# Kernel optimization log

Hardware: AMD Instinct MI355X
Metric: run time of the kernel (lower is better)

Reference implementation:

```python
import jax, jax.numpy as jnp
import numpy as np

N_NODES = 100000
N_EDGES = 3200000
IN_DIM, HID, OUT_DIM = 512, 64, 5


def _glorot(key, shape):
    fan_in, fan_out = shape[0], shape[1]
    lim = np.sqrt(6.0 / (fan_in + fan_out))
    return jax.random.uniform(key, shape, jnp.float32, -lim, lim)


def setup_inputs() -> dict:
    key = jax.random.key(0)
    ks = jax.random.split(key, 10)
    x = jax.random.normal(ks[0], (N_NODES, IN_DIM), jnp.float32)
    edge_index = jax.random.randint(ks[1], (2, N_EDGES), 0, N_NODES, jnp.int64)
    edge_weight = jax.random.uniform(ks[2], (N_EDGES,), jnp.float32)
    return {
        "x": x,
        "edge_index": edge_index,
        "edge_weight": edge_weight,
        "W1": _glorot(ks[3], (IN_DIM, HID)),
        "b1": jnp.zeros((HID,), jnp.float32),
        "W2": _glorot(ks[4], (HID, HID)),
        "b2": jnp.zeros((HID,), jnp.float32),
        "Wfc": _glorot(ks[5], (HID, OUT_DIM)),
        "bfc": jnp.zeros((OUT_DIM,), jnp.float32),
    }


def _gcn_norm(edge_index, edge_weight, num_nodes):
    # PyG gcn_norm: add self-loops (weight 1), symmetric deg^-1/2 normalization.
    loop = jnp.arange(num_nodes, dtype=edge_index.dtype)
    src = jnp.concatenate([edge_index[0], loop])
    dst = jnp.concatenate([edge_index[1], loop])
    ew = jnp.concatenate([edge_weight, jnp.ones((num_nodes,), edge_weight.dtype)])
    deg = jax.ops.segment_sum(ew, dst, num_segments=num_nodes)
    dinv = jnp.where(deg > 0, jax.lax.rsqrt(deg), 0.0)
    norm = dinv[src] * ew * dinv[dst]
    return src, dst, norm


def _gcn_conv(x, W, b, src, dst, norm, num_nodes):
    h = x @ W  # transform first (GCNConv does lin before propagate)
    msg = norm[:, None] * h[src]  # gather + scale  [E, d]
    out = jax.ops.segment_sum(msg, dst, num_segments=num_nodes)  # scatter-add
    return out + b


def reference(x, edge_index, edge_weight, W1, b1, W2, b2, Wfc, bfc):
    n = x.shape[0]
    src, dst, norm = _gcn_norm(edge_index, edge_weight, n)
    h = jax.nn.relu(_gcn_conv(x, W1, b1, src, dst, norm, n))
    h = jax.nn.relu(_gcn_conv(h, W2, b2, src, dst, norm, n))
    return h @ Wfc + bfc
```

## Files before the change

### kernel.cpp

```cpp
#include <hip/hip_runtime.h>

#define IN_DIM 512
#define HID 64
#define OUT_DIM 5


__device__ __forceinline__ unsigned short f2bf(float f) {
    unsigned u = __float_as_uint(f);
    u += 0x7FFF + ((u >> 16) & 1);
    return (unsigned short)(u >> 16);
}
__device__ __forceinline__ float bf2f(unsigned short b) {
    return __uint_as_float(((unsigned)b) << 16);
}


__global__ void k_init(unsigned long long* __restrict__ packed, int n) {
    int i = blockIdx.x * blockDim.x + threadIdx.x;
    if (i < n) packed[i] = 0ULL;
}


__global__ void k_hist4(const int* __restrict__ dst, const float* __restrict__ ew,
                        unsigned long long* __restrict__ packed, int* __restrict__ rank, int nE) {
    int base = (blockIdx.x * blockDim.x + threadIdx.x) * 4;
    if (base + 3 < nE) {
        int4   d4 = *(const int4*)&dst[base];
        float4 w4 = *(const float4*)&ew[base];
        unsigned long long f0 = (unsigned long long)(w4.x * 4294967296.0);
        unsigned long long f1 = (unsigned long long)(w4.y * 4294967296.0);
        unsigned long long f2 = (unsigned long long)(w4.z * 4294967296.0);
        unsigned long long f3 = (unsigned long long)(w4.w * 4294967296.0);
        unsigned long long o0 = atomicAdd(&packed[d4.x], (1ULL << 44) | f0);
        unsigned long long o1 = atomicAdd(&packed[d4.y], (1ULL << 44) | f1);
        unsigned long long o2 = atomicAdd(&packed[d4.z], (1ULL << 44) | f2);
        unsigned long long o3 = atomicAdd(&packed[d4.w], (1ULL << 44) | f3);
        int4 r4;
        r4.x = (int)(o0 >> 44);
        r4.y = (int)(o1 >> 44);
        r4.z = (int)(o2 >> 44);
        r4.w = (int)(o3 >> 44);
        *(int4*)&rank[base] = r4;
    } else {
        for (int e = base; e < nE; ++e) {
            int d = dst[e];
            unsigned long long fx = (unsigned long long)(ew[e] * 4294967296.0);
            unsigned long long old = atomicAdd(&packed[d], (1ULL << 44) | fx);
            rank[e] = (int)(old >> 44);
        }
    }
}


__global__ void k_dinv(const unsigned long long* __restrict__ packed,
                       float* __restrict__ dinv, int* __restrict__ cnt, int n) {
    int i = blockIdx.x * blockDim.x + threadIdx.x;
    if (i < n) {
        unsigned long long p = packed[i];
        int c = (int)(p >> 44);
        double ewsum = (double)(p & ((1ULL << 44) - 1)) * (1.0 / 4294967296.0);
        float deg = 1.0f + (float)ewsum;
        dinv[i] = rsqrtf(deg);
        cnt[i] = c;
    }
}


__global__ void k_scan1(const int* __restrict__ cnt, int* __restrict__ rowptr,
                        int* __restrict__ bsum, int n) {
    __shared__ int sdata[256];
    int t = threadIdx.x, b = blockIdx.x;
    int base = b * 1024 + t * 4;
    int v[4], s = 0;
#pragma unroll
    for (int k = 0; k < 4; ++k) { int i = base + k; v[k] = (i < n) ? cnt[i] : 0; s += v[k]; }
    sdata[t] = s;
    __syncthreads();
    int x = s;
    for (int off = 1; off < 256; off <<= 1) {
        int y = (t >= off) ? sdata[t - off] : 0;
        __syncthreads();
        x += y;
        sdata[t] = x;
        __syncthreads();
    }
    int run = x - s;
    if (t == 255) bsum[b] = x;
#pragma unroll
    for (int k = 0; k < 4; ++k) { int i = base + k; if (i < n) rowptr[i] = run; run += v[k]; }
}

__global__ void k_scan2(int* __restrict__ bsum, int nb) {
    __shared__ int sdata[256];
    int t = threadIdx.x;
    int s = (t < nb) ? bsum[t] : 0;
    sdata[t] = s;
    __syncthreads();
    int x = s;
    for (int off = 1; off < 256; off <<= 1) {
        int y = (t >= off) ? sdata[t - off] : 0;
        __syncthreads();
        x += y;
        sdata[t] = x;
        __syncthreads();
    }
    if (t < nb) bsum[t] = x - s;
}

__global__ void k_scan3(int* __restrict__ rowptr, const int* __restrict__ bsum, int n, int E) {
    int i = blockIdx.x * blockDim.x + threadIdx.x;
    if (i < n) rowptr[i] += bsum[i >> 10];
    else if (i == n) rowptr[n] = E;
}


__global__ void k_reorder(const int* __restrict__ src, const int* __restrict__ dst,
                          const float* __restrict__ ew, const float* __restrict__ dinv,
                          const int* __restrict__ rowptr, const int* __restrict__ rank,
                          int2* __restrict__ edges, int nE) {
    int e = blockIdx.x * blockDim.x + threadIdx.x;
    if (e < nE) {
        int s = src[e];
        int d = dst[e];
        float w = dinv[s] * ew[e] * dinv[d];
        int pos = rowptr[d] + rank[e];
        edges[pos] = make_int2(s, __float_as_int(w));
    }
}


__launch_bounds__(256)
__global__ void k_aggregate(const float* __restrict__ h, const unsigned short* __restrict__ hb,
                            const float* __restrict__ dinv,
                            const int2* __restrict__ edges, const int* __restrict__ rowptr,
                            float* __restrict__ out, int N) {
    int n = (blockIdx.x * 256 + threadIdx.x) >> 6;
    int lane = threadIdx.x & 63;
    if (n >= N) return;

    float dn = dinv[n];
    float acc = dn * dn * h[(size_t)n * HID + lane];

    int beg = rowptr[n], end = rowptr[n + 1];
    int j = beg;
    for (; j + 7 < end; j += 8) {
        int2 p0 = edges[j];
        int2 p1 = edges[j + 1];
        int2 p2 = edges[j + 2];
        int2 p3 = edges[j + 3];
        int2 p4 = edges[j + 4];
        int2 p5 = edges[j + 5];
        int2 p6 = edges[j + 6];
        int2 p7 = edges[j + 7];
        float h0 = bf2f(hb[(size_t)p0.x * HID + lane]);
        float h1 = bf2f(hb[(size_t)p1.x * HID + lane]);
        float h2 = bf2f(hb[(size_t)p2.x * HID + lane]);
        float h3 = bf2f(hb[(size_t)p3.x * HID + lane]);
        float h4 = bf2f(hb[(size_t)p4.x * HID + lane]);
        float h5 = bf2f(hb[(size_t)p5.x * HID + lane]);
        float h6 = bf2f(hb[(size_t)p6.x * HID + lane]);
        float h7 = bf2f(hb[(size_t)p7.x * HID + lane]);
        acc = fmaf(__int_as_float(p0.y), h0, acc);
        acc = fmaf(__int_as_float(p1.y), h1, acc);
        acc = fmaf(__int_as_float(p2.y), h2, acc);
        acc = fmaf(__int_as_float(p3.y), h3, acc);
        acc = fmaf(__int_as_float(p4.y), h4, acc);
        acc = fmaf(__int_as_float(p5.y), h5, acc);
        acc = fmaf(__int_as_float(p6.y), h6, acc);
        acc = fmaf(__int_as_float(p7.y), h7, acc);
    }
    for (; j < end; ++j) {
        int2 p = edges[j];
        acc = fmaf(__int_as_float(p.y), bf2f(hb[(size_t)p.x * HID + lane]), acc);
    }
    out[(size_t)n * HID + lane] = acc;
}


template <int K_, bool RELU_BIAS>
__launch_bounds__(256)
__global__ void k_gemm_n64(const float* __restrict__ A, const float* __restrict__ W,
                           const float* __restrict__ bias, float* __restrict__ out,
                           unsigned short* __restrict__ outb, int M) {
    constexpr int BK = 16;
    __shared__ float As[BK][68];
    __shared__ float Ws[BK][64];

    const int t  = threadIdx.x;
    const int tx = t & 15;
    const int ty = t >> 4;
    const int row0 = blockIdx.x * 64;

    const int lr = t >> 2;
    const int lk = (t & 3) * 4;

    float acc[4][4] = {};

    for (int k0 = 0; k0 < K_; k0 += BK) {
        float4 av = make_float4(0.f, 0.f, 0.f, 0.f);
        int ar = row0 + lr;
        if (ar < M) {
            av = *(const float4*)&A[(long long)ar * K_ + k0 + lk];
            if (RELU_BIAS) {
                const float4 bv = *(const float4*)&bias[k0 + lk];
                av.x = fmaxf(av.x + bv.x, 0.f);
                av.y = fmaxf(av.y + bv.y, 0.f);
                av.z = fmaxf(av.z + bv.z, 0.f);
                av.w = fmaxf(av.w + bv.w, 0.f);
            }
        }
        As[lk + 0][lr] = av.x;
        As[lk + 1][lr] = av.y;
        As[lk + 2][lr] = av.z;
        As[lk + 3][lr] = av.w;

        *(float4*)&Ws[t >> 4][(t & 15) * 4] =
            *(const float4*)&W[(long long)(k0 + (t >> 4)) * 64 + (t & 15) * 4];

        __syncthreads();

#pragma unroll
        for (int kk = 0; kk < BK; ++kk) {
            float4 a4 = *(const float4*)&As[kk][ty * 4];
            float4 b4 = *(const float4*)&Ws[kk][tx * 4];
            float a[4] = {a4.x, a4.y, a4.z, a4.w};
            float b[4] = {b4.x, b4.y, b4.z, b4.w};
#pragma unroll
            for (int i = 0; i < 4; ++i)
#pragma unroll
                for (int j = 0; j < 4; ++j)
                    acc[i][j] = fmaf(a[i], b[j], acc[i][j]);
        }
        __syncthreads();
    }

#pragma unroll
    for (int i = 0; i < 4; ++i) {
        int r = row0 + ty * 4 + i;
        if (r < M) {
            *(float4*)&out[(long long)r * 64 + tx * 4] =
                make_float4(acc[i][0], acc[i][1], acc[i][2], acc[i][3]);
            ushort4 hv;
            hv.x = f2bf(acc[i][0]);
            hv.y = f2bf(acc[i][1]);
            hv.z = f2bf(acc[i][2]);
            hv.w = f2bf(acc[i][3]);
            *(ushort4*)&outb[(long long)r * 64 + tx * 4] = hv;
        }
    }
}


__launch_bounds__(256)
__global__ void k_final(const float* __restrict__ agg, const float* __restrict__ b2,
                        const float* __restrict__ Wfc, const float* __restrict__ bfc,
                        float* __restrict__ out, int N) {
    __shared__ float Wsf[HID * OUT_DIM];
    __shared__ float bs[HID];
    int t = threadIdx.x;
    for (int i = t; i < HID * OUT_DIM; i += 256) Wsf[i] = Wfc[i];
    if (t < HID) bs[t] = b2[t];
    __syncthreads();

    int n = blockIdx.x * blockDim.x + t;
    if (n >= N) return;

    float acc[OUT_DIM];
#pragma unroll
    for (int o = 0; o < OUT_DIM; ++o) acc[o] = bfc[o];

    const float4* ag = (const float4*)&agg[(long long)n * HID];
#pragma unroll
    for (int k4 = 0; k4 < HID / 4; ++k4) {
        float4 v4 = ag[k4];
        float v[4] = {v4.x, v4.y, v4.z, v4.w};
#pragma unroll
        for (int j = 0; j < 4; ++j) {
            int k = k4 * 4 + j;
            float f = fmaxf(v[j] + bs[k], 0.f);
#pragma unroll
            for (int o = 0; o < OUT_DIM; ++o)
                acc[o] = fmaf(f, Wsf[k * OUT_DIM + o], acc[o]);
        }
    }
#pragma unroll
    for (int o = 0; o < OUT_DIM; ++o) out[(long long)n * OUT_DIM + o] = acc[o];
}


static inline size_t align_up(size_t x, size_t a) { return (x + a - 1) & ~(a - 1); }

extern "C" void kernel_launch(void* const* d_in, const int* in_sizes, int n_in,
                              void* d_out, int out_size, void* d_ws, size_t ws_size,
                              hipStream_t stream) {
    const float* x   = (const float*)d_in[0];
    const int*   ei  = (const int*)d_in[1];
    const float* ew  = (const float*)d_in[2];
    const float* W1  = (const float*)d_in[3];
    const float* b1  = (const float*)d_in[4];
    const float* W2  = (const float*)d_in[5];
    const float* b2  = (const float*)d_in[6];
    const float* Wfc = (const float*)d_in[7];
    const float* bfc = (const float*)d_in[8];
    float* out = (float*)d_out;

    const int E = in_sizes[2];
    const int N = in_sizes[0] / IN_DIM;
    const int* src = ei;
    const int* dst = ei + E;

    char* p = (char*)d_ws;
    unsigned long long* packed = (unsigned long long*)p; p += align_up((size_t)N * 8, 256);
    float* dinv   = (float*)p;  p += align_up((size_t)N * 4, 256);
    int*   cnt    = (int*)p;    p += align_up((size_t)N * 4, 256);
    int*   rowptr = (int*)p;    p += align_up((size_t)(N + 1) * 4, 256);
    int*   bsum   = (int*)p;    p += align_up((size_t)256 * 4, 256);
    int*   rank   = (int*)p;    p += align_up((size_t)E * 4, 256);
    unsigned short* hb = (unsigned short*)rank;
    int2*  edges  = (int2*)p;   p += align_up((size_t)E * 8, 256);
    float* bufA   = (float*)p;  p += align_up((size_t)N * HID * 4, 256);
    float* bufB   = (float*)p;  p += align_up((size_t)N * HID * 4, 256);
    (void)ws_size; (void)n_in; (void)out_size;

    const int BS = 256;
    dim3 blk(BS);
    int gN  = (N + BS - 1) / BS;
    int gN1 = (N + 1 + BS - 1) / BS;
    int gE  = (E + BS - 1) / BS;
    int gE4 = (E + BS * 4 - 1) / (BS * 4);
    int gM  = (N + 63) / 64;
    int nb  = (N + 1023) / 1024;
    int gAg = (N + 3) / 4;

    k_init<<<gN, blk, 0, stream>>>(packed, N);
    k_hist4<<<gE4, blk, 0, stream>>>(dst, ew, packed, rank, E);
    k_dinv<<<gN, blk, 0, stream>>>(packed, dinv, cnt, N);
    k_scan1<<<nb, blk, 0, stream>>>(cnt, rowptr, bsum, N);
    k_scan2<<<1, blk, 0, stream>>>(bsum, nb);
    k_scan3<<<gN1, blk, 0, stream>>>(rowptr, bsum, N, E);
    k_reorder<<<gE, blk, 0, stream>>>(src, dst, ew, dinv, rowptr, rank, edges, E);

    k_gemm_n64<IN_DIM, false><<<gM, blk, 0, stream>>>(x, W1, nullptr, bufA, hb, N);
    k_aggregate<<<gAg, blk, 0, stream>>>(bufA, hb, dinv, edges, rowptr, bufB, N);

    k_gemm_n64<HID, true><<<gM, blk, 0, stream>>>(bufB, W2, b1, bufA, hb, N);
    k_aggregate<<<gAg, blk, 0, stream>>>(bufA, hb, dinv, edges, rowptr, bufB, N);

    k_final<<<gN, blk, 0, stream>>>(bufB, b2, Wfc, bfc, out, N);
}
```

Measured before the change: 822.4 us.

## Run first GEMM concurrently with degree histogram in one launch; fuse dinv into scan

Merges the layer-1 X·W1 GEMM and the atomic degree/rank histogram into a single launch, split by block index, so the compute-bound GEMM and the atomic-bound histogram can overlap on the GPU. It also folds the dinv computation into the first scan pass, which removes one kernel and the cnt buffer. The workspace is rearranged so that rank lives in bufB and hb gets its own region, since the GEMM now writes hb while rank is still live. The cost is that the GEMM blocks and the atomic blocks now compete for the same compute units and cache.

```diff
diff --git a/kernel.cpp b/kernel.cpp
--- a/kernel.cpp
+++ b/kernel.cpp
@@ -21,59 +21,122 @@
 }
 
 
-__global__ void k_hist4(const int* __restrict__ dst, const float* __restrict__ ew,
-                        unsigned long long* __restrict__ packed, int* __restrict__ rank, int nE) {
-    int base = (blockIdx.x * blockDim.x + threadIdx.x) * 4;
-    if (base + 3 < nE) {
-        int4   d4 = *(const int4*)&dst[base];
-        float4 w4 = *(const float4*)&ew[base];
-        unsigned long long f0 = (unsigned long long)(w4.x * 4294967296.0);
-        unsigned long long f1 = (unsigned long long)(w4.y * 4294967296.0);
-        unsigned long long f2 = (unsigned long long)(w4.z * 4294967296.0);
-        unsigned long long f3 = (unsigned long long)(w4.w * 4294967296.0);
-        unsigned long long o0 = atomicAdd(&packed[d4.x], (1ULL << 44) | f0);
-        unsigned long long o1 = atomicAdd(&packed[d4.y], (1ULL << 44) | f1);
-        unsigned long long o2 = atomicAdd(&packed[d4.z], (1ULL << 44) | f2);
-        unsigned long long o3 = atomicAdd(&packed[d4.w], (1ULL << 44) | f3);
-        int4 r4;
-        r4.x = (int)(o0 >> 44);
-        r4.y = (int)(o1 >> 44);
-        r4.z = (int)(o2 >> 44);
-        r4.w = (int)(o3 >> 44);
-        *(int4*)&rank[base] = r4;
+__launch_bounds__(256)
+__global__ void k_gemm1_hist(const float* __restrict__ A, const float* __restrict__ W,
+                             float* __restrict__ out, unsigned short* __restrict__ outb, int M,
+                             const int* __restrict__ dst, const float* __restrict__ ew,
+                             unsigned long long* __restrict__ packed, int* __restrict__ rank,
+                             int nE, int gemmBlocks) {
+    if ((int)blockIdx.x < gemmBlocks) {
+        constexpr int K_ = IN_DIM;
+        constexpr int BK = 16;
+        __shared__ float As[BK][68];
+        __shared__ float Ws[BK][64];
+
+        const int t  = threadIdx.x;
+        const int tx = t & 15;
+        const int ty = t >> 4;
+        const int row0 = blockIdx.x * 64;
+
+        const int lr = t >> 2;
+        const int lk = (t & 3) * 4;
+
+        float acc[4][4] = {};
+
+        for (int k0 = 0; k0 < K_; k0 += BK) {
+            float4 av = make_float4(0.f, 0.f, 0.f, 0.f);
+            int ar = row0 + lr;
+            if (ar < M) av = *(const float4*)&A[(long long)ar * K_ + k0 + lk];
+            As[lk + 0][lr] = av.x;
+            As[lk + 1][lr] = av.y;
+            As[lk + 2][lr] = av.z;
+            As[lk + 3][lr] = av.w;
+
+            *(float4*)&Ws[t >> 4][(t & 15) * 4] =
+                *(const float4*)&W[(long long)(k0 + (t >> 4)) * 64 + (t & 15) * 4];
+
+            __syncthreads();
+
+#pragma unroll
+            for (int kk = 0; kk < BK; ++kk) {
+                float4 a4 = *(const float4*)&As[kk][ty * 4];
+                float4 b4 = *(const float4*)&Ws[kk][tx * 4];
+                float a[4] = {a4.x, a4.y, a4.z, a4.w};
+                float b[4] = {b4.x, b4.y, b4.z, b4.w};
+#pragma unroll
+                for (int i = 0; i < 4; ++i)
+#pragma unroll
+                    for (int j = 0; j < 4; ++j)
+                        acc[i][j] = fmaf(a[i], b[j], acc[i][j]);
+            }
+            __syncthreads();
+        }
+
+#pragma unroll
+        for (int i = 0; i < 4; ++i) {
+            int r = row0 + ty * 4 + i;
+            if (r < M) {
+                *(float4*)&out[(long long)r * 64 + tx * 4] =
+                    make_float4(acc[i][0], acc[i][1], acc[i][2], acc[i][3]);
+                ushort4 hv;
+                hv.x = f2bf(acc[i][0]);
+                hv.y = f2bf(acc[i][1]);
+                hv.z = f2bf(acc[i][2]);
+                hv.w = f2bf(acc[i][3]);
+                *(ushort4*)&outb[(long long)r * 64 + tx * 4] = hv;
+            }
+        }
     } else {
-        for (int e = base; e < nE; ++e) {
-            int d = dst[e];
-            unsigned long long fx = (unsigned long long)(ew[e] * 4294967296.0);
-            unsigned long long old = atomicAdd(&packed[d], (1ULL << 44) | fx);
-            rank[e] = (int)(old >> 44);
-        }
-    }
-}
-
-
-__global__ void k_dinv(const unsigned long long* __restrict__ packed,
-                       float* __restrict__ dinv, int* __restrict__ cnt, int n) {
-    int i = blockIdx.x * blockDim.x + threadIdx.x;
-    if (i < n) {
-        unsigned long long p = packed[i];
-        int c = (int)(p >> 44);
-        double ewsum = (double)(p & ((1ULL << 44) - 1)) * (1.0 / 4294967296.0);
-        float deg = 1.0f + (float)ewsum;
-        dinv[i] = rsqrtf(deg);
-        cnt[i] = c;
-    }
-}
-
-
-__global__ void k_scan1(const int* __restrict__ cnt, int* __restrict__ rowptr,
-                        int* __restrict__ bsum, int n) {
+        int base = ((blockIdx.x - gemmBlocks) * 256 + threadIdx.x) * 4;
+        if (base + 3 < nE) {
+            int4   d4 = *(const int4*)&dst[base];
+            float4 w4 = *(const float4*)&ew[base];
+            unsigned long long f0 = (unsigned long long)(w4.x * 4294967296.0);
+            unsigned long long f1 = (unsigned long long)(w4.y * 4294967296.0);
+            unsigned long long f2 = (unsigned long long)(w4.z * 4294967296.0);
+            unsigned long long f3 = (unsigned long long)(w4.w * 4294967296.0);
+            unsigned long long o0 = atomicAdd(&packed[d4.x], (1ULL << 44) | f0);
+            unsigned long long o1 = atomicAdd(&packed[d4.y], (1ULL << 44) | f1);
+            unsigned long long o2 = atomicAdd(&packed[d4.z], (1ULL << 44) | f2);
+            unsigned long long o3 = atomicAdd(&packed[d4.w], (1ULL << 44) | f3);
+            int4 r4;
+            r4.x = (int)(o0 >> 44);
+            r4.y = (int)(o1 >> 44);
+            r4.z = (int)(o2 >> 44);
+            r4.w = (int)(o3 >> 44);
+            *(int4*)&rank[base] = r4;
+        } else {
+            for (int e = base; e < nE; ++e) {
+                int d = dst[e];
+                unsigned long long fx = (unsigned long long)(ew[e] * 4294967296.0);
+                unsigned long long old = atomicAdd(&packed[d], (1ULL << 44) | fx);
+                rank[e] = (int)(old >> 44);
+            }
+        }
+    }
+}
+
+
+__global__ void k_scan1d(const unsigned long long* __restrict__ packed,
+                         float* __restrict__ dinv, int* __restrict__ rowptr,
+                         int* __restrict__ bsum, int n) {
     __shared__ int sdata[256];
     int t = threadIdx.x, b = blockIdx.x;
     int base = b * 1024 + t * 4;
     int v[4], s = 0;
 #pragma unroll
-    for (int k = 0; k < 4; ++k) { int i = base + k; v[k] = (i < n) ? cnt[i] : 0; s += v[k]; }
+    for (int k = 0; k < 4; ++k) {
+        int i = base + k;
+        int c = 0;
+        if (i < n) {
+            unsigned long long p = packed[i];
+            c = (int)(p >> 44);
+            double ewsum = (double)(p & ((1ULL << 44) - 1)) * (1.0 / 4294967296.0);
+            dinv[i] = rsqrtf(1.0f + (float)ewsum);
+        }
+        v[k] = c;
+        s += c;
+    }
     sdata[t] = s;
     __syncthreads();
     int x = s;
@@ -312,14 +375,13 @@
     char* p = (char*)d_ws;
     unsigned long long* packed = (unsigned long long*)p; p += align_up((size_t)N * 8, 256);
     float* dinv   = (float*)p;  p += align_up((size_t)N * 4, 256);
-    int*   cnt    = (int*)p;    p += align_up((size_t)N * 4, 256);
     int*   rowptr = (int*)p;    p += align_up((size_t)(N + 1) * 4, 256);
     int*   bsum   = (int*)p;    p += align_up((size_t)256 * 4, 256);
-    int*   rank   = (int*)p;    p += align_up((size_t)E * 4, 256);
-    unsigned short* hb = (unsigned short*)rank;
+    unsigned short* hb = (unsigned short*)p; p += align_up((size_t)N * HID * 2, 256);
     int2*  edges  = (int2*)p;   p += align_up((size_t)E * 8, 256);
     float* bufA   = (float*)p;  p += align_up((size_t)N * HID * 4, 256);
     float* bufB   = (float*)p;  p += align_up((size_t)N * HID * 4, 256);
+    int*   rank   = (int*)bufB;
     (void)ws_size; (void)n_in; (void)out_size;
 
     const int BS = 256;
@@ -333,14 +395,13 @@
     int gAg = (N + 3) / 4;
 
     k_init<<<gN, blk, 0, stream>>>(packed, N);
-    k_hist4<<<gE4, blk, 0, stream>>>(dst, ew, packed, rank, E);
-    k_dinv<<<gN, blk, 0, stream>>>(packed, dinv, cnt, N);
-    k_scan1<<<nb, blk, 0, stream>>>(cnt, rowptr, bsum, N);
+    k_gemm1_hist<<<gM + gE4, blk, 0, stream>>>(x, W1, bufA, hb, N,
+                                               dst, ew, packed, rank, E, gM);
+    k_scan1d<<<nb, blk, 0, stream>>>(packed, dinv, rowptr, bsum, N);
     k_scan2<<<1, blk, 0, stream>>>(bsum, nb);
     k_scan3<<<gN1, blk, 0, stream>>>(rowptr, bsum, N, E);
     k_reorder<<<gE, blk, 0, stream>>>(src, dst, ew, dinv, rowptr, rank, edges, E);
 
-    k_gemm_n64<IN_DIM, false><<<gM, blk, 0, stream>>>(x, W1, nullptr, bufA, hb, N);
     k_aggregate<<<gAg, blk, 0, stream>>>(bufA, hb, dinv, edges, rowptr, bufB, N);
 
     k_gemm_n64<HID, true><<<gM, blk, 0, stream>>>(bufB, W2, b1, bufA, hb, N);
```

Measured after the change: 748.0 us. -9.0%, faster.

## Fuse GEMM1 with histogram, aggregate with GEMM2, aggregate with final projection

Applied to the files above, without the earlier changes.

The first GEMM and the degree histogram now run as one launch, with separate block ranges for each, so the compute-bound and atomic-bound work can overlap. The dinv computation is folded into the first scan pass. Each aggregation kernel now applies bias, ReLU and the next dense layer in place: the 64x64 W2 is read from shared memory with wave shuffles, and the 64x5 FC uses xor reductions. This drops the standalone GEMM2 and final kernels and their global round trips, at the cost of extra per-block shared memory and shuffle work inside the gather kernels.

```diff
diff --git a/kernel.cpp b/kernel.cpp
--- a/kernel.cpp
+++ b/kernel.cpp
@@ -21,59 +21,122 @@
 }
 
 
-__global__ void k_hist4(const int* __restrict__ dst, const float* __restrict__ ew,
-                        unsigned long long* __restrict__ packed, int* __restrict__ rank, int nE) {
-    int base = (blockIdx.x * blockDim.x + threadIdx.x) * 4;
-    if (base + 3 < nE) {
-        int4   d4 = *(const int4*)&dst[base];
-        float4 w4 = *(const float4*)&ew[base];
-        unsigned long long f0 = (unsigned long long)(w4.x * 4294967296.0);
-        unsigned long long f1 = (unsigned long long)(w4.y * 4294967296.0);
-        unsigned long long f2 = (unsigned long long)(w4.z * 4294967296.0);
-        unsigned long long f3 = (unsigned long long)(w4.w * 4294967296.0);
-        unsigned long long o0 = atomicAdd(&packed[d4.x], (1ULL << 44) | f0);
-        unsigned long long o1 = atomicAdd(&packed[d4.y], (1ULL << 44) | f1);
-        unsigned long long o2 = atomicAdd(&packed[d4.z], (1ULL << 44) | f2);
-        unsigned long long o3 = atomicAdd(&packed[d4.w], (1ULL << 44) | f3);
-        int4 r4;
-        r4.x = (int)(o0 >> 44);
-        r4.y = (int)(o1 >> 44);
-        r4.z = (int)(o2 >> 44);
-        r4.w = (int)(o3 >> 44);
-        *(int4*)&rank[base] = r4;
+__launch_bounds__(256)
+__global__ void k_gemm1_hist(const float* __restrict__ A, const float* __restrict__ W,
+                             float* __restrict__ out, unsigned short* __restrict__ outb, int M,
+                             const int* __restrict__ dst, const float* __restrict__ ew,
+                             unsigned long long* __restrict__ packed, int* __restrict__ rank,
+                             int nE, int gemmBlocks) {
+    if ((int)blockIdx.x < gemmBlocks) {
+        constexpr int K_ = IN_DIM;
+        constexpr int BK = 16;
+        __shared__ float As[BK][68];
+        __shared__ float Ws[BK][64];
+
+        const int t  = threadIdx.x;
+        const int tx = t & 15;
+        const int ty = t >> 4;
+        const int row0 = blockIdx.x * 64;
+
+        const int lr = t >> 2;
+        const int lk = (t & 3) * 4;
+
+        float acc[4][4] = {};
+
+        for (int k0 = 0; k0 < K_; k0 += BK) {
+            float4 av = make_float4(0.f, 0.f, 0.f, 0.f);
+            int ar = row0 + lr;
+            if (ar < M) av = *(const float4*)&A[(long long)ar * K_ + k0 + lk];
+            As[lk + 0][lr] = av.x;
+            As[lk + 1][lr] = av.y;
+            As[lk + 2][lr] = av.z;
+            As[lk + 3][lr] = av.w;
+
+            *(float4*)&Ws[t >> 4][(t & 15) * 4] =
+                *(const float4*)&W[(long long)(k0 + (t >> 4)) * 64 + (t & 15) * 4];
+
+            __syncthreads();
+
+#pragma unroll
+            for (int kk = 0; kk < BK; ++kk) {
+                float4 a4 = *(const float4*)&As[kk][ty * 4];
+                float4 b4 = *(const float4*)&Ws[kk][tx * 4];
+                float a[4] = {a4.x, a4.y, a4.z, a4.w};
+                float b[4] = {b4.x, b4.y, b4.z, b4.w};
+#pragma unroll
+                for (int i = 0; i < 4; ++i)
+#pragma unroll
+                    for (int j = 0; j < 4; ++j)
+                        acc[i][j] = fmaf(a[i], b[j], acc[i][j]);
+            }
+            __syncthreads();
+        }
+
+#pragma unroll
+        for (int i = 0; i < 4; ++i) {
+            int r = row0 + ty * 4 + i;
+            if (r < M) {
+                *(float4*)&out[(long long)r * 64 + tx * 4] =
+                    make_float4(acc[i][0], acc[i][1], acc[i][2], acc[i][3]);
+                ushort4 hv;
+                hv.x = f2bf(acc[i][0]);
+                hv.y = f2bf(acc[i][1]);
+                hv.z = f2bf(acc[i][2]);
+                hv.w = f2bf(acc[i][3]);
+                *(ushort4*)&outb[(long long)r * 64 + tx * 4] = hv;
+            }
+        }
     } else {
-        for (int e = base; e < nE; ++e) {
-            int d = dst[e];
-            unsigned long long fx = (unsigned long long)(ew[e] * 4294967296.0);
-            unsigned long long old = atomicAdd(&packed[d], (1ULL << 44) | fx);
-            rank[e] = (int)(old >> 44);
+        int base = ((blockIdx.x - gemmBlocks) * 256 + threadIdx.x) * 4;
+        if (base + 3 < nE) {
+            int4   d4 = *(const int4*)&dst[base];
+            float4 w4 = *(const float4*)&ew[base];
+            unsigned long long f0 = (unsigned long long)(w4.x * 4294967296.0);
+            unsigned long long f1 = (unsigned long long)(w4.y * 4294967296.0);
+            unsigned long long f2 = (unsigned long long)(w4.z * 4294967296.0);
+            unsigned long long f3 = (unsigned long long)(w4.w * 4294967296.0);
+            unsigned long long o0 = atomicAdd(&packed[d4.x], (1ULL << 44) | f0);
+            unsigned long long o1 = atomicAdd(&packed[d4.y], (1ULL << 44) | f1);
+            unsigned long long o2 = atomicAdd(&packed[d4.z], (1ULL << 44) | f2);
+            unsigned long long o3 = atomicAdd(&packed[d4.w], (1ULL << 44) | f3);
+            int4 r4;
+            r4.x = (int)(o0 >> 44);
+            r4.y = (int)(o1 >> 44);
+            r4.z = (int)(o2 >> 44);
+            r4.w = (int)(o3 >> 44);
+            *(int4*)&rank[base] = r4;
+        } else {
+            for (int e = base; e < nE; ++e) {
+                int d = dst[e];
+                unsigned long long fx = (unsigned long long)(ew[e] * 4294967296.0);
+                unsigned long long old = atomicAdd(&packed[d], (1ULL << 44) | fx);
+                rank[e] = (int)(old >> 44);
+            }
         }
     }
 }
 
 
-__global__ void k_dinv(const unsigned long long* __restrict__ packed,
-                       float* __restrict__ dinv, int* __restrict__ cnt, int n) {
-    int i = blockIdx.x * blockDim.x + threadIdx.x;
-    if (i < n) {
-        unsigned long long p = packed[i];
-        int c = (int)(p >> 44);
-        double ewsum = (double)(p & ((1ULL << 44) - 1)) * (1.0 / 4294967296.0);
-        float deg = 1.0f + (float)ewsum;
-        dinv[i] = rsqrtf(deg);
-        cnt[i] = c;
-    }
-}
-
-
-__global__ void k_scan1(const int* __restrict__ cnt, int* __restrict__ rowptr,
-                        int* __restrict__ bsum, int n) {
+__global__ void k_scan1d(const unsigned long long* __restrict__ packed,
+                         float* __restrict__ dinv, int* __restrict__ rowptr,
+                         int* __restrict__ bsum, int n) {
     __shared__ int sdata[256];
     int t = threadIdx.x, b = blockIdx.x;
     int base = b * 1024 + t * 4;
     int v[4], s = 0;
 #pragma unroll
-    for (int k = 0; k < 4; ++k) { int i = base + k; v[k] = (i < n) ? cnt[i] : 0; s += v[k]; }
+    for (int k = 0; k < 4; ++k) {
+        int i = base + k;
+        int c = 0;
+        if (i < n) {
+            unsigned long long p = packed[i];
+            c = (int)(p >> 44);
+            double ewsum = (double)(p & ((1ULL << 44) - 1)) * (1.0 / 4294967296.0);
+            dinv[i] = rsqrtf(1.0f + (float)ewsum);
+        }
+        v[k] = c;
+        s += c;
+    }
     sdata[t] = s;
     __syncthreads();
     int x = s;
@@ -130,12 +193,21 @@
 
 
 __launch_bounds__(256)
-__global__ void k_aggregate(const float* __restrict__ h, const unsigned short* __restrict__ hb,
+__global__ void k_agg_gemm2(const float* __restrict__ h, const unsigned short* __restrict__ hb,
                             const float* __restrict__ dinv,
                             const int2* __restrict__ edges, const int* __restrict__ rowptr,
-                            float* __restrict__ out, int N) {
-    int n = (blockIdx.x * 256 + threadIdx.x) >> 6;
-    int lane = threadIdx.x & 63;
+                            const float* __restrict__ b1, const float* __restrict__ W2,
+                            float* __restrict__ h2, unsigned short* __restrict__ hb2, int N) {
+    __shared__ float W2s[HID][HID];
+    __shared__ float b1s[HID];
+    const int t = threadIdx.x;
+    for (int i = t * 4; i < HID * HID; i += 256 * 4)
+        *(float4*)&W2s[0][i] = *(const float4*)&W2[i];
+    if (t < HID) b1s[t] = b1[t];
+    __syncthreads();
+
+    int n = (blockIdx.x * 256 + t) >> 6;
+    int lane = t & 63;
     if (n >= N) return;
 
     float dn = dinv[n];
@@ -154,7 +226,7 @@
         int2 p7 = edges[j + 7];
         float h0 = bf2f(hb[(size_t)p0.x * HID + lane]);
         float h1 = bf2f(hb[(size_t)p1.x * HID + lane]);
-        float h2 = bf2f(hb[(size_t)p2.x * HID + lane]);
+        float h2v = bf2f(hb[(size_t)p2.x * HID + lane]);
         float h3 = bf2f(hb[(size_t)p3.x * HID + lane]);
         float h4 = bf2f(hb[(size_t)p4.x * HID + lane]);
         float h5 = bf2f(hb[(size_t)p5.x * HID + lane]);
@@ -162,7 +234,7 @@
         float h7 = bf2f(hb[(size_t)p7.x * HID + lane]);
         acc = fmaf(__int_as_float(p0.y), h0, acc);
         acc = fmaf(__int_as_float(p1.y), h1, acc);
-        acc = fmaf(__int_as_float(p2.y), h2, acc);
+        acc = fmaf(__int_as_float(p2.y), h2v, acc);
         acc = fmaf(__int_as_float(p3.y), h3, acc);
         acc = fmaf(__int_as_float(p4.y), h4, acc);
         acc = fmaf(__int_as_float(p5.y), h5, acc);
@@ -173,118 +245,88 @@
         int2 p = edges[j];
         acc = fmaf(__int_as_float(p.y), bf2f(hb[(size_t)p.x * HID + lane]), acc);
     }
-    out[(size_t)n * HID + lane] = acc;
-}
-
-
-template <int K_, bool RELU_BIAS>
+
+    float f = fmaxf(acc + b1s[lane], 0.f);
+    float o = 0.f;
+#pragma unroll
+    for (int k = 0; k < HID; ++k)
+        o = fmaf(__shfl(f, k, 64), W2s[k][lane], o);
+
+    h2[(size_t)n * HID + lane] = o;
+    hb2[(size_t)n * HID + lane] = f2bf(o);
+}
+
+
 __launch_bounds__(256)
-__global__ void k_gemm_n64(const float* __restrict__ A, const float* __restrict__ W,
-                           const float* __restrict__ bias, float* __restrict__ out,
-                           unsigned short* __restrict__ outb, int M) {
-    constexpr int BK = 16;
-    __shared__ float As[BK][68];
-    __shared__ float Ws[BK][64];
-
-    const int t  = threadIdx.x;
-    const int tx = t & 15;
-    const int ty = t >> 4;
-    const int row0 = blockIdx.x * 64;
-
-    const int lr = t >> 2;
-    const int lk = (t & 3) * 4;
-
-    float acc[4][4] = {};
-
-    for (int k0 = 0; k0 < K_; k0 += BK) {
-        float4 av = make_float4(0.f, 0.f, 0.f, 0.f);
-        int ar = row0 + lr;
-        if (ar < M) {
-            av = *(const float4*)&A[(long long)ar * K_ + k0 + lk];
-            if (RELU_BIAS) {
-                const float4 bv = *(const float4*)&bias[k0 + lk];
-                av.x = fmaxf(av.x + bv.x, 0.f);
-                av.y = fmaxf(av.y + bv.y, 0.f);
-                av.z = fmaxf(av.z + bv.z, 0.f);
-                av.w = fmaxf(av.w + bv.w, 0.f);
-            }
-        }
-        As[lk + 0][lr] = av.x;
-        As[lk + 1][lr] = av.y;
-        As[lk + 2][lr] = av.z;
-        As[lk + 3][lr] = av.w;
-
-        *(float4*)&Ws[t >> 4][(t & 15) * 4] =
-            *(const float4*)&W[(long long)(k0 + (t >> 4)) * 64 + (t & 15) * 4];
-
-        __syncthreads();
-
-#pragma unroll
-        for (int kk = 0; kk < BK; ++kk) {
-            float4 a4 = *(const float4*)&As[kk][ty * 4];
-            float4 b4 = *(const float4*)&Ws[kk][tx * 4];
-            float a[4] = {a4.x, a4.y, a4.z, a4.w};
-            float b[4] = {b4.x, b4.y, b4.z, b4.w};
-#pragma unroll
-            for (int i = 0; i < 4; ++i)
-#pragma unroll
-                for (int j = 0; j < 4; ++j)
-                    acc[i][j] = fmaf(a[i], b[j], acc[i][j]);
-        }
-        __syncthreads();
-    }
-
-#pragma unroll
-    for (int i = 0; i < 4; ++i) {
-        int r = row0 + ty * 4 + i;
-        if (r < M) {
-            *(float4*)&out[(long long)r * 64 + tx * 4] =
-                make_float4(acc[i][0], acc[i][1], acc[i][2], acc[i][3]);
-            ushort4 hv;
-            hv.x = f2bf(acc[i][0]);
-            hv.y = f2bf(acc[i][1]);
-            hv.z = f2bf(acc[i][2]);
-            hv.w = f2bf(acc[i][3]);
-            *(ushort4*)&outb[(long long)r * 64 + tx * 4] = hv;
-        }
-    }
-}
-
-
-__launch_bounds__(256)
-__global__ void k_final(const float* __restrict__ agg, const float* __restrict__ b2,
-                        const float* __restrict__ Wfc, const float* __restrict__ bfc,
-                        float* __restrict__ out, int N) {
-    __shared__ float Wsf[HID * OUT_DIM];
-    __shared__ float bs[HID];
-    int t = threadIdx.x;
-    for (int i = t; i < HID * OUT_DIM; i += 256) Wsf[i] = Wfc[i];
-    if (t < HID) bs[t] = b2[t];
+__global__ void k_agg_final(const float* __restrict__ h, const unsigned short* __restrict__ hb,
+                            const float* __restrict__ dinv,
+                            const int2* __restrict__ edges, const int* __restrict__ rowptr,
+                            const float* __restrict__ b2, const float* __restrict__ Wfc,
+                            const float* __restrict__ bfc, float* __restrict__ out, int N) {
+    __shared__ float Wfs[HID * OUT_DIM];
+    __shared__ float b2s[HID];
+    __shared__ float bfcs[OUT_DIM];
+    const int t = threadIdx.x;
+    for (int i = t; i < HID * OUT_DIM; i += 256) Wfs[i] = Wfc[i];
+    if (t < HID) b2s[t] = b2[t];
+    if (t < OUT_DIM) bfcs[t] = bfc[t];
     __syncthreads();
 
-    int n = blockIdx.x * blockDim.x + t;
+    int n = (blockIdx.x * 256 + t) >> 6;
+    int lane = t & 63;
     if (n >= N) return;
 
-    float acc[OUT_DIM];
-#pragma unroll
-    for (int o = 0; o < OUT_DIM; ++o) acc[o] = bfc[o];
-
-    const float4* ag = (const float4*)&agg[(long long)n * HID];
-#pragma unroll
-    for (int k4 = 0; k4 < HID / 4; ++k4) {
-        float4 v4 = ag[k4];
-        float v[4] = {v4.x, v4.y, v4.z, v4.w};
-#pragma unroll
-        for (int j = 0; j < 4; ++j) {
-            int k = k4 * 4 + j;
-            float f = fmaxf(v[j] + bs[k], 0.f);
-#pragma unroll
-            for (int o = 0; o < OUT_DIM; ++o)
-                acc[o] = fmaf(f, Wsf[k * OUT_DIM + o], acc[o]);
-        }
-    }
-#pragma unroll
-    for (int o = 0; o < OUT_DIM; ++o) out[(long long)n * OUT_DIM + o] = acc[o];
+    float dn = dinv[n];
+    float acc = dn * dn * h[(size_t)n * HID + lane];
+
+    int beg = rowptr[n], end = rowptr[n + 1];
+    int j = beg;
+    for (; j + 7 < end; j += 8) {
+        int2 p0 = edges[j];
+        int2 p1 = edges[j + 1];
+        int2 p2 = edges[j + 2];
+        int2 p3 = edges[j + 3];
+        int2 p4 = edges[j + 4];
+        int2 p5 = edges[j + 5];
+        int2 p6 = edges[j + 6];
+        int2 p7 = edges[j + 7];
+        float h0 = bf2f(hb[(size_t)p0.x * HID + lane]);
+        float h1 = bf2f(hb[(size_t)p1.x * HID + lane]);
+        float h2v = bf2f(hb[(size_t)p2.x * HID + lane]);
+        float h3 = bf2f(hb[(size_t)p3.x * HID + lane]);
+        float h4 = bf2f(hb[(size_t)p4.x * HID + lane]);
+        float h5 = bf2f(hb[(size_t)p5.x * HID + lane]);
+        float h6 = bf2f(hb[(size_t)p6.x * HID + lane]);
+        float h7 = bf2f(hb[(size_t)p7.x * HID + lane]);
+        acc = fmaf(__int_as_float(p0.y), h0, acc);
+        acc = fmaf(__int_as_float(p1.y), h1, acc);
+        acc = fmaf(__int_as_float(p2.y), h2v, acc);
+        acc = fmaf(__int_as_float(p3.y), h3, acc);
+        acc = fmaf(__int_as_float(p4.y), h4, acc);
+        acc = fmaf(__int_as_float(p5.y), h5, acc);
+        acc = fmaf(__int_as_float(p6.y), h6, acc);
+        acc = fmaf(__int_as_float(p7.y), h7, acc);
+    }
+    for (; j < end; ++j) {
+        int2 p = edges[j];
+        acc = fmaf(__int_as_float(p.y), bf2f(hb[(size_t)p.x * HID + lane]), acc);
+    }
+
+    float f = fmaxf(acc + b2s[lane], 0.f);
+    float vo[OUT_DIM];
+#pragma unroll
+    for (int o = 0; o < OUT_DIM; ++o) {
+        float v = f * Wfs[lane * OUT_DIM + o];
+#pragma unroll
+        for (int off = 32; off >= 1; off >>= 1)
+            v += __shfl_xor(v, off, 64);
+        vo[o] = v;
+    }
+    if (lane == 0) {
+#pragma unroll
+        for (int o = 0; o < OUT_DIM; ++o)
+            out[(size_t)n * OUT_DIM + o] = vo[o] + bfcs[o];
+    }
 }
 
 
@@ -312,14 +354,15 @@
     char* p = (char*)d_ws;
     unsigned long long* packed = (unsigned long long*)p; p += align_up((size_t)N * 8, 256);
     float* dinv   = (float*)p;  p += align_up((size_t)N * 4, 256);
-    int*   cnt    = (int*)p;    p += align_up((size_t)N * 4, 256);
     int*   rowptr = (int*)p;    p += align_up((size_t)(N + 1) * 4, 256);
     int*   bsum   = (int*)p;    p += align_up((size_t)256 * 4, 256);
-    int*   rank   = (int*)p;    p += align_up((size_t)E * 4, 256);
-    unsigned short* hb = (unsigned short*)rank;
+    unsigned short* hb1 = (unsigned short*)p; p += align_up((size_t)N * HID * 2, 256);
     int2*  edges  = (int2*)p;   p += align_up((size_t)E * 8, 256);
     float* bufA   = (float*)p;  p += align_up((size_t)N * HID * 4, 256);
     float* bufB   = (float*)p;  p += align_up((size_t)N * HID * 4, 256);
+    int*   rank   = (int*)p;
+    unsigned short* hb2 = (unsigned short*)p;
+    p += align_up((size_t)E * 4, 256);
     (void)ws_size; (void)n_in; (void)out_size;
 
     const int BS = 256;
@@ -333,18 +376,16 @@
     int gAg = (N + 3) / 4;
 
     k_init<<<gN, blk, 0, stream>>>(packed, N);
-    k_hist4<<<gE4, blk, 0, stream>>>(dst, ew, packed, rank, E);
-    k_dinv<<<gN, blk, 0, stream>>>(packed, dinv, cnt, N);
-    k_scan1<<<nb, blk, 0, stream>>>(cnt, rowptr, bsum, N);
+    k_gemm1_hist<<<gM + gE4, blk, 0, stream>>>(x, W1, bufA, hb1, N,
+                                               dst, ew, packed, rank, E, gM);
+    k_scan1d<<<nb, blk, 0, stream>>>(packed, dinv, rowptr, bsum, N);
     k_scan2<<<1, blk, 0, stream>>>(bsum, nb);
     k_scan3<<<gN1, blk, 0, stream>>>(rowptr, bsum, N, E);
     k_reorder<<<gE, blk, 0, stream>>>(src, dst, ew, dinv, rowptr, rank, edges, E);
 
-    k_gemm_n64<IN_DIM, false><<<gM, blk, 0, stream>>>(x, W1, nullptr, bufA, hb, N);
-    k_aggregate<<<gAg, blk, 0, stream>>>(bufA, hb, dinv, edges, rowptr, bufB, N);
-
-    k_gemm_n64<HID, true><<<gM, blk, 0, stream>>>(bufB, W2, b1, bufA, hb, N);
-    k_aggregate<<<gAg, blk, 0, stream>>>(bufA, hb, dinv, edges, rowptr, bufB, N);
-
-    k_final<<<gN, blk, 0, stream>>>(bufB, b2, Wfc, bfc, out, N);
-}
+    k_agg_gemm2<<<gAg, blk, 0, stream>>>(bufA, hb1, dinv, edges, rowptr,
+                                         b1, W2, bufB, hb2, N);
+
+    k_agg_final<<<gAg, blk, 0, stream>>>(bufB, hb2, dinv, edges, rowptr,
+                                         b2, Wfc, bfc, out, N);
+}
```

Measured after the change: 797.0 us. 1.03x faster.
